# Kernel tuning notes

Hardware: AMD Instinct MI355X
Metric: run time of the kernel (lower is better)

Reference implementation:

```python
import jax, jax.numpy as jnp
import numpy as np

L = 3        # layer_num
D = 64       # hidden_size (input_dim)
NU = 100000  # user nodes in batched graph
NI = 100000  # item nodes in batched graph
NUSER = 200000  # user vocab
NITEM = 200000  # item vocab
E = 1000000  # edges per relation ('by' and 'pby')
B = 1024     # target users per batch


def _time_enc(t, freq, phase):
    # TimeEncode: cos(t * basis_freq + phase), per edge -> [E, D]
    return jnp.cos(t[:, None] * freq[None, :] + phase[None, :])


def _seg_attn(e, vals, dst, num_seg):
    # softmax of e over edges sharing a destination node, then weighted sum of vals
    m = jax.ops.segment_max(e, dst, num_segments=num_seg)
    ex = jnp.exp(e - m[dst])
    denom = jax.ops.segment_sum(ex, dst, num_segments=num_seg)
    alpha = ex / denom[dst]
    return jax.ops.segment_sum(alpha[:, None] * vals, dst, num_segments=num_seg)


def _forward(user_emb, item_emb, Wu, Wi, Wuu, Wii,
             u_freq, u_phase, uk_freq, uk_phase,
             i_freq, i_phase, ik_freq, ik_phase,
             unified_W, dense_W, dense_b,
             by_time, pby_time,
             user_id, item_id, by_src, by_dst, pby_src, pby_dst,
             user_index, last_item_index):
    nu = user_id.shape[0]
    ni = item_id.shape[0]
    d = user_emb.shape[1]
    scale = 1.0 / jnp.sqrt(jnp.float32(d))
    user_h = user_emb[user_id]   # [NU, D]
    item_h = item_emb[item_id]   # [NI, D]
    user_layers = []
    n_layers = Wu.shape[0]
    for l in range(n_layers):
        uh = user_h @ Wu[l]   # user_weight
        ih = item_h @ Wi[l]   # item_weight
        # --- 'by' relation: item -> user (user_reduce_func) ---
        src_i = ih[by_src]    # mailbox['item_h']
        dst_u = uh[by_dst]    # mailbox['user_h'] (dst feature)
        e_u = jnp.sum((_time_enc(by_time, u_freq[l], u_phase[l]) + src_i) * dst_u, -1) * scale
        agg_u = _seg_attn(e_u, src_i + _time_enc(by_time, uk_freq[l], uk_phase[l]), by_dst, nu)
        # --- 'pby' relation: user -> item (item_reduce_func) ---
        src_u = uh[pby_src]
        dst_i = ih[pby_dst]
        e_i = jnp.sum((_time_enc(pby_time, i_freq[l], i_phase[l]) + src_u) * dst_i, -1) * scale
        agg_i = _seg_attn(e_i, src_u + _time_enc(pby_time, ik_freq[l], ik_phase[l]), pby_dst, ni)
        # node update: elu(W [agg ; old])
        user_h = jax.nn.elu(jnp.concatenate([agg_u, user_h], -1) @ Wuu[l])
        item_h = jax.nn.elu(jnp.concatenate([agg_i, item_h], -1) @ Wii[l])
        user_layers.append(user_h[user_index])
    user_layers.append(item_h[last_item_index])  # last_item=True
    unified = jnp.concatenate(user_layers, -1) @ unified_W
    return jax.nn.relu(unified @ dense_W + dense_b)  # [B, 3]


def setup_inputs() -> dict:
    key = jax.random.key(0)
    ks = jax.random.split(key, 20)
    w = lambda k, shape: jax.random.normal(k, shape, jnp.float32) * 0.05
    freq0 = jnp.asarray(1.0 / 10 ** np.linspace(0, 9, D), dtype=jnp.float32)
    freq = jnp.tile(freq0[None], (L, 1))
    zph = jnp.zeros((L, D), jnp.float32)
    return {
        'user_emb': w(ks[0], (NUSER, D)),
        'item_emb': w(ks[1], (NITEM, D)),
        'Wu': w(ks[2], (L, D, D)),
        'Wi': w(ks[3], (L, D, D)),
        'Wuu': w(ks[4], (L, 2 * D, D)),
        'Wii': w(ks[5], (L, 2 * D, D)),
        'u_freq': freq, 'u_phase': zph,
        'uk_freq': freq, 'uk_phase': zph,
        'i_freq': freq, 'i_phase': zph,
        'ik_freq': freq, 'ik_phase': zph,
        'unified_W': w(ks[6], ((L + 1) * D, D)),
        'dense_W': w(ks[7], (D, 3)),
        'dense_b': jnp.zeros((3,), jnp.float32),
        'by_time': jax.random.uniform(ks[8], (E,), jnp.float32),
        'pby_time': jax.random.uniform(ks[9], (E,), jnp.float32),
        'user_id': jax.random.randint(ks[10], (NU,), 0, NUSER),
        'item_id': jax.random.randint(ks[11], (NI,), 0, NITEM),
        'by_src': jax.random.randint(ks[12], (E,), 0, NI),
        'by_dst': jax.random.randint(ks[13], (E,), 0, NU),
        'pby_src': jax.random.randint(ks[14], (E,), 0, NU),
        'pby_dst': jax.random.randint(ks[15], (E,), 0, NI),
        'user_index': jax.random.randint(ks[16], (B,), 0, NU),
        'last_item_index': jax.random.randint(ks[17], (B,), 0, NI),
    }


def reference(user_emb, item_emb, Wu, Wi, Wuu, Wii,
              u_freq, u_phase, uk_freq, uk_phase,
              i_freq, i_phase, ik_freq, ik_phase,
              unified_W, dense_W, dense_b,
              by_time, pby_time,
              user_id, item_id, by_src, by_dst, pby_src, pby_dst,
              user_index, last_item_index):
    return _forward(user_emb, item_emb, Wu, Wi, Wuu, Wii,
                    u_freq, u_phase, uk_freq, uk_phase,
                    i_freq, i_phase, ik_freq, ik_phase,
                    unified_W, dense_W, dense_b,
                    by_time, pby_time,
                    user_id, item_id, by_src, by_dst, pby_src, pby_dst,
                    user_index, last_item_index)
```

## Files before the change

### kernel.cpp

```cpp
#include <hip/hip_runtime.h>
#include <math.h>

#define D 64

typedef __attribute__((ext_vector_type(8))) short s8bf;
typedef __attribute__((ext_vector_type(4))) float fx4;

__device__ __forceinline__ float bf2f(unsigned short u) {
    union { unsigned int i; float f; } v; v.i = ((unsigned int)u) << 16; return v.f;
}
__device__ __forceinline__ unsigned short f2bf(float f) {
    union { float f; unsigned int i; } v; v.f = f;
    unsigned int r = v.i + 0x7FFFu + ((v.i >> 16) & 1u);
    return (unsigned short)(r >> 16);
}

__global__ __launch_bounds__(256) void k_gather2(const float* __restrict__ ue,
                                                 const float* __restrict__ ie,
                                                 const int* __restrict__ uid,
                                                 const int* __restrict__ iid,
                                                 unsigned short* __restrict__ uh0,
                                                 unsigned short* __restrict__ ih0, int NU, int NI) {
    int i = blockIdx.x * blockDim.x + threadIdx.x;
    if (i >= (NU + NI) * D) return;
    int r = i >> 6, c = i & 63;
    if (r < NU) uh0[(size_t)r * D + c] = f2bf(ue[(size_t)uid[r] * D + c]);
    else { int j = r - NU; ih0[(size_t)j * D + c] = f2bf(ie[(size_t)iid[j] * D + c]); }
}

__global__ __launch_bounds__(256) void k_wprep(const float* __restrict__ Wu,
                                               const float* __restrict__ Wi,
                                               const float* __restrict__ Wuu,
                                               const float* __restrict__ Wii,
                                               unsigned short* __restrict__ WuT,
                                               unsigned short* __restrict__ WiT,
                                               unsigned short* __restrict__ WuuT,
                                               unsigned short* __restrict__ WiiT, int L) {
    int i = blockIdx.x * blockDim.x + threadIdx.x;
    int n1 = L * 64 * 64, n2 = L * 64 * 128;
    if (i < n1) {
        int l = i >> 12, c = (i >> 6) & 63, k = i & 63;
        WuT[i] = f2bf(Wu[l * 4096 + k * 64 + c]);
        WiT[i] = f2bf(Wi[l * 4096 + k * 64 + c]);
    }
    if (i < n2) {
        int l = i >> 13, c = (i >> 7) & 63, k = i & 127;
        WuuT[i] = f2bf(Wuu[l * 8192 + k * 64 + c]);
        WiiT[i] = f2bf(Wii[l * 8192 + k * 64 + c]);
    }
}

__global__ __launch_bounds__(256) void k_hist2(const int* __restrict__ bd,
                                               const int* __restrict__ pd,
                                               int* __restrict__ cu, int* __restrict__ ci, int E) {
    for (int i = blockIdx.x * blockDim.x + threadIdx.x; i < 2 * E; i += gridDim.x * blockDim.x) {
        if (i < E) atomicAdd(&cu[bd[i]], 1);
        else       atomicAdd(&ci[pd[i - E]], 1);
    }
}

__global__ __launch_bounds__(256) void k_scan_block2(const int* __restrict__ cu, int* __restrict__ rp_u,
                                                     const int* __restrict__ ci, int* __restrict__ rp_i,
                                                     int* __restrict__ bsums, int nbU, int NU, int NI) {
    __shared__ int ts[256];
    bool rel = blockIdx.x >= (unsigned)nbU;
    const int* in = rel ? ci : cu;
    int* out = rel ? rp_i : rp_u;
    int n = rel ? NI : NU;
    int boff = rel ? blockIdx.x - nbU : blockIdx.x;
    int t = threadIdx.x;
    int base = boff * 2048 + t * 8;
    int v[8]; int s = 0;
#pragma unroll
    for (int k = 0; k < 8; ++k) { int idx = base + k; v[k] = idx < n ? in[idx] : 0; s += v[k]; }
    ts[t] = s; __syncthreads();
    for (int off = 1; off < 256; off <<= 1) {
        int x = (t >= off) ? ts[t - off] : 0;
        __syncthreads(); ts[t] += x; __syncthreads();
    }
    int excl = ts[t] - s;
    if (t == 255) bsums[blockIdx.x] = ts[255];
    int run = excl;
#pragma unroll
    for (int k = 0; k < 8; ++k) { int idx = base + k; if (idx < n) out[idx] = run; run += v[k]; }
}

__global__ __launch_bounds__(256) void k_scan_small(int* __restrict__ bsums, int nbU, int nbI) {
    __shared__ int ts[256];
    int t = threadIdx.x;
    int half = t >> 7, local = t & 127;
    int nb = half ? nbI : nbU;
    int g = half ? nbU + local : local;
    int v = local < nb ? bsums[g] : 0;
    ts[t] = v; __syncthreads();
    for (int off = 1; off < 128; off <<= 1) {
        int x = (local >= off) ? ts[t - off] : 0;
        __syncthreads(); ts[t] += x; __syncthreads();
    }
    if (local < nb) bsums[g] = ts[t] - v;
}

__global__ __launch_bounds__(256) void k_fixup2(int* __restrict__ rp_u, int* __restrict__ rp_i,
                                                const int* __restrict__ bsums,
                                                int* __restrict__ cu, int* __restrict__ ci,
                                                int NU, int NI, int E, int nbU) {
    int i = blockIdx.x * blockDim.x + threadIdx.x;
    if (i < NU) {
        int v = rp_u[i] + bsums[i >> 11]; rp_u[i] = v; cu[i] = v;
        if (i == 0) rp_u[NU] = E;
    } else if (i < NU + NI) {
        int j = i - NU;
        int v = rp_i[j] + bsums[nbU + (j >> 11)]; rp_i[j] = v; ci[j] = v;
        if (j == 0) rp_i[NI] = E;
    }
}

__global__ __launch_bounds__(256) void k_scatter2(
    const int* __restrict__ bs, const int* __restrict__ bd, const float* __restrict__ bt,
    const int* __restrict__ ps, const int* __restrict__ pd, const float* __restrict__ pt,
    int* __restrict__ cu, int* __restrict__ ci,
    int4* __restrict__ be, int4* __restrict__ pe, int E) {
    for (int i = blockIdx.x * blockDim.x + threadIdx.x; i < 2 * E; i += gridDim.x * blockDim.x) {
        if (i < E) {
            int d = bd[i]; int pos = atomicAdd(&cu[d], 1);
            be[pos] = make_int4(bs[i], __float_as_int(bt[i]), d, 0);
        } else {
            int k = i - E;
            int d = pd[k]; int pos = atomicAdd(&ci[d], 1);
            pe[pos] = make_int4(ps[k], __float_as_int(pt[k]), d, 0);
        }
    }
}

__global__ __launch_bounds__(256) void k_transform4(
    const unsigned short* __restrict__ user_h, const unsigned short* __restrict__ item_h,
    const unsigned short* __restrict__ WuT_l, const unsigned short* __restrict__ WiT_l,
    unsigned short* __restrict__ uh, unsigned short* __restrict__ ih,
    int NU, int NI, int G) {
    bool rel = blockIdx.x >= (unsigned)G;
    int b = rel ? blockIdx.x - G : blockIdx.x;
    const unsigned short* in = rel ? item_h : user_h;
    const unsigned short* WT = rel ? WiT_l : WuT_l;
    unsigned short* out = rel ? ih : uh;
    int n = rel ? NI : NU;
    int lane = threadIdx.x & 63;
    int l15 = lane & 15, l4 = lane >> 4;
    s8bf bfr[8];
#pragma unroll
    for (int ct = 0; ct < 4; ++ct)
#pragma unroll
        for (int kk = 0; kk < 2; ++kk)
            bfr[ct * 2 + kk] = *(const s8bf*)&WT[(ct * 16 + l15) * 64 + kk * 32 + l4 * 8];
    int wave = b * 4 + (threadIdx.x >> 6);
    int nw = G * 4;
    int ntiles = (n + 15) >> 4;
    for (int t = wave; t < ntiles; t += nw) {
        int r = t * 16 + l15; if (r >= n) r = n - 1;
        s8bf afr0 = *(const s8bf*)&in[(size_t)r * 64 + l4 * 8];
        s8bf afr1 = *(const s8bf*)&in[(size_t)r * 64 + 32 + l4 * 8];
#pragma unroll
        for (int ct = 0; ct < 4; ++ct) {
            fx4 c = {0.f, 0.f, 0.f, 0.f};
            c = __builtin_amdgcn_mfma_f32_16x16x32_bf16(afr0, bfr[ct * 2 + 0], c, 0, 0, 0);
            c = __builtin_amdgcn_mfma_f32_16x16x32_bf16(afr1, bfr[ct * 2 + 1], c, 0, 0, 0);
#pragma unroll
            for (int i2 = 0; i2 < 4; ++i2) {
                int row = t * 16 + l4 * 4 + i2;
                if (row < n) out[(size_t)row * 64 + ct * 16 + l15] = f2bf(c[i2]);
            }
        }
    }
}

__global__ __launch_bounds__(256) void k_edge2(
    const unsigned short* __restrict__ ihF, const unsigned short* __restrict__ uhF,
    const int4* __restrict__ by_e, const int4* __restrict__ pby_e,
    const float* __restrict__ uf, const float* __restrict__ up,
    const float* __restrict__ ukf, const float* __restrict__ ukp,
    const float* __restrict__ ifq, const float* __restrict__ ipq,
    const float* __restrict__ ikf, const float* __restrict__ ikp,
    float* __restrict__ agg_u, float* __restrict__ den_u,
    float* __restrict__ agg_i, float* __restrict__ den_i,
    int E, int EB) {
    bool rel = blockIdx.x >= (unsigned)EB;
    int rblk = rel ? blockIdx.x - EB : blockIdx.x;
    const unsigned short* srcF = rel ? uhF : ihF;
    const unsigned short* dstF = rel ? ihF : uhF;
    const int4* ee = rel ? pby_e : by_e;
    const float* efq = rel ? ifq : uf;
    const float* eps = rel ? ipq : up;
    const float* kfq = rel ? ikf : ukf;
    const float* kps = rel ? ikp : ukp;
    float* agg = rel ? agg_i : agg_u;
    float* den = rel ? den_i : den_u;

    int lane = threadIdx.x & 15;
    int grp  = threadIdx.x >> 4;
    int base = rblk * 256 + grp * 16;
    if (base >= E) return;
    float ef0 = efq[lane], ef1 = efq[lane + 16], ef2 = efq[lane + 32], ef3 = efq[lane + 48];
    float ep0 = eps[lane], ep1 = eps[lane + 16], ep2 = eps[lane + 32], ep3 = eps[lane + 48];
    float kf0 = kfq[lane], kf1 = kfq[lane + 16], kf2 = kfq[lane + 32], kf3 = kfq[lane + 48];
    float kp0 = kps[lane], kp1 = kps[lane + 16], kp2 = kps[lane + 32], kp3 = kps[lane + 48];
    bool same = ef0 == kf0 && ef1 == kf1 && ef2 == kf2 && ef3 == kf3 &&
                ep0 == kp0 && ep1 == kp1 && ep2 == kp2 && ep3 == kp3;
    same = __all(same);

    float a0 = 0, a1 = 0, a2 = 0, a3 = 0, dn = 0;
    float d0 = 0, d1 = 0, d2 = 0, d3 = 0;
    int cur = -1;
    for (int j = 0; j < 16; ++j) {
        int e = base + j;
        if (e >= E) break;
        int4 q = ee[e];
        int s = q.x; float t = __int_as_float(q.y); int dd = q.z;
        if (dd != cur) {
            if (cur >= 0) {
                float* ap = &agg[(size_t)cur * D + lane];
                unsafeAtomicAdd(ap +  0, a0); unsafeAtomicAdd(ap + 16, a1);
                unsafeAtomicAdd(ap + 32, a2); unsafeAtomicAdd(ap + 48, a3);
                if (lane == 0) unsafeAtomicAdd(&den[cur], dn);
            }
            a0 = a1 = a2 = a3 = 0; dn = 0; cur = dd;
            const unsigned short* dp = &dstF[(size_t)dd * D + lane];
            d0 = bf2f(dp[0]); d1 = bf2f(dp[16]); d2 = bf2f(dp[32]); d3 = bf2f(dp[48]);
        }
        const unsigned short* sp = &srcF[(size_t)s * D + lane];
        float s0 = bf2f(sp[0]), s1 = bf2f(sp[16]), s2 = bf2f(sp[32]), s3 = bf2f(sp[48]);
        float c0 = __cosf(fmaf(t, ef0, ep0));
        float c1 = __cosf(fmaf(t, ef1, ep1));
        float c2 = __cosf(fmaf(t, ef2, ep2));
        float c3 = __cosf(fmaf(t, ef3, ep3));
        float p = (c0 + s0) * d0 + (c1 + s1) * d1 + (c2 + s2) * d2 + (c3 + s3) * d3;
        p += __shfl_xor(p, 1); p += __shfl_xor(p, 2);
        p += __shfl_xor(p, 4); p += __shfl_xor(p, 8);
        float ex = __expf(p * 0.125f);
        float k0, k1, k2, k3;
        if (same) { k0 = c0; k1 = c1; k2 = c2; k3 = c3; }
        else {
            k0 = __cosf(fmaf(t, kf0, kp0)); k1 = __cosf(fmaf(t, kf1, kp1));
            k2 = __cosf(fmaf(t, kf2, kp2)); k3 = __cosf(fmaf(t, kf3, kp3));
        }
        a0 = fmaf(ex, s0 + k0, a0); a1 = fmaf(ex, s1 + k1, a1);
        a2 = fmaf(ex, s2 + k2, a2); a3 = fmaf(ex, s3 + k3, a3);
        dn += ex;
    }
    if (cur >= 0) {
        float* ap = &agg[(size_t)cur * D + lane];
        unsafeAtomicAdd(ap +  0, a0); unsafeAtomicAdd(ap + 16, a1);
        unsafeAtomicAdd(ap + 32, a2); unsafeAtomicAdd(ap + 48, a3);
        if (lane == 0) unsafeAtomicAdd(&den[cur], dn);
    }
}

__global__ __launch_bounds__(256) void k_update4(
    unsigned short* __restrict__ user_h, unsigned short* __restrict__ item_h,
    const float* __restrict__ agg_u, const float* __restrict__ den_u,
    const float* __restrict__ agg_i, const float* __restrict__ den_i,
    const unsigned short* __restrict__ WuuT_l, const unsigned short* __restrict__ WiiT_l,
    int NU, int NI, int G) {
    bool rel = blockIdx.x >= (unsigned)G;
    int b = rel ? blockIdx.x - G : blockIdx.x;
    unsigned short* h = rel ? item_h : user_h;
    const float* agg = rel ? agg_i : agg_u;
    const float* den = rel ? den_i : den_u;
    const unsigned short* WT = rel ? WiiT_l : WuuT_l;
    int n = rel ? NI : NU;
    int lane = threadIdx.x & 63;
    int l15 = lane & 15, l4 = lane >> 4;
    s8bf bfr[16];
#pragma unroll
    for (int ct = 0; ct < 4; ++ct)
#pragma unroll
        for (int kk = 0; kk < 4; ++kk)
            bfr[ct * 4 + kk] = *(const s8bf*)&WT[(ct * 16 + l15) * 128 + kk * 32 + l4 * 8];
    int wave = b * 4 + (threadIdx.x >> 6);
    int nw = G * 4;
    int ntiles = (n + 15) >> 4;
    for (int t = wave; t < ntiles; t += nw) {
        int r = t * 16 + l15; if (r >= n) r = n - 1;
        float dd = den[r];
        float inv = dd > 0.f ? 1.f / dd : 0.f;
        s8bf afr[4];
#pragma unroll
        for (int kk = 0; kk < 2; ++kk) {
            const float4* ap = (const float4*)&agg[(size_t)r * 64 + kk * 32 + l4 * 8];
            float4 x = ap[0], y = ap[1];
            s8bf f;
            f[0] = (short)f2bf(x.x * inv); f[1] = (short)f2bf(x.y * inv);
            f[2] = (short)f2bf(x.z * inv); f[3] = (short)f2bf(x.w * inv);
            f[4] = (short)f2bf(y.x * inv); f[5] = (short)f2bf(y.y * inv);
            f[6] = (short)f2bf(y.z * inv); f[7] = (short)f2bf(y.w * inv);
            afr[kk] = f;
        }
        afr[2] = *(const s8bf*)&h[(size_t)r * 64 + l4 * 8];
        afr[3] = *(const s8bf*)&h[(size_t)r * 64 + 32 + l4 * 8];
#pragma unroll
        for (int ct = 0; ct < 4; ++ct) {
            fx4 c = {0.f, 0.f, 0.f, 0.f};
            c = __builtin_amdgcn_mfma_f32_16x16x32_bf16(afr[0], bfr[ct * 4 + 0], c, 0, 0, 0);
            c = __builtin_amdgcn_mfma_f32_16x16x32_bf16(afr[1], bfr[ct * 4 + 1], c, 0, 0, 0);
            c = __builtin_amdgcn_mfma_f32_16x16x32_bf16(afr[2], bfr[ct * 4 + 2], c, 0, 0, 0);
            c = __builtin_amdgcn_mfma_f32_16x16x32_bf16(afr[3], bfr[ct * 4 + 3], c, 0, 0, 0);
#pragma unroll
            for (int i2 = 0; i2 < 4; ++i2) {
                int row = t * 16 + l4 * 4 + i2;
                if (row < n) {
                    float o = c[i2];
                    h[(size_t)row * 64 + ct * 16 + l15] =
                        f2bf(o > 0.f ? o : __expf(o) - 1.f);
                }
            }
        }
    }
}

__global__ __launch_bounds__(256) void k_gather_feat(const unsigned short* __restrict__ h,
                                                     const int* __restrict__ idx,
                                                     float* __restrict__ feat, int B,
                                                     int colOff, int FW) {
    int i = blockIdx.x * blockDim.x + threadIdx.x;
    if (i >= B * D) return;
    int b = i >> 6, c = i & 63;
    feat[(size_t)b * FW + colOff + c] = bf2f(h[(size_t)idx[b] * D + c]);
}

__global__ __launch_bounds__(64) void k_final(const float* __restrict__ feat,
                                              const float* __restrict__ uW,
                                              const float* __restrict__ dW,
                                              const float* __restrict__ db,
                                              float* __restrict__ out, int B, int FW) {
    __shared__ float fr[512];
    __shared__ float un[D];
    int b = blockIdx.x;
    int c = threadIdx.x;
    for (int i = c; i < FW; i += 64) fr[i] = feat[(size_t)b * FW + i];
    __syncthreads();
    float acc = 0.f;
    for (int d = 0; d < FW; ++d) acc += fr[d] * uW[d * D + c];
    un[c] = acc;
    __syncthreads();
    if (c < 3) {
        float o = db[c];
#pragma unroll
        for (int d = 0; d < D; ++d) o += un[d] * dW[d * 3 + c];
        out[b * 3 + c] = o > 0.f ? o : 0.f;
    }
}

extern "C" void kernel_launch(void* const* d_in, const int* in_sizes, int n_in,
                              void* d_out, int out_size, void* d_ws, size_t ws_size,
                              hipStream_t stream) {
    const float* user_emb = (const float*)d_in[0];
    const float* item_emb = (const float*)d_in[1];
    const float* Wu       = (const float*)d_in[2];
    const float* Wi       = (const float*)d_in[3];
    const float* Wuu      = (const float*)d_in[4];
    const float* Wii      = (const float*)d_in[5];
    const float* u_freq   = (const float*)d_in[6];
    const float* u_phase  = (const float*)d_in[7];
    const float* uk_freq  = (const float*)d_in[8];
    const float* uk_phase = (const float*)d_in[9];
    const float* i_freq   = (const float*)d_in[10];
    const float* i_phase  = (const float*)d_in[11];
    const float* ik_freq  = (const float*)d_in[12];
    const float* ik_phase = (const float*)d_in[13];
    const float* unified_W = (const float*)d_in[14];
    const float* dense_W   = (const float*)d_in[15];
    const float* dense_b   = (const float*)d_in[16];
    const float* by_time   = (const float*)d_in[17];
    const float* pby_time  = (const float*)d_in[18];
    const int* user_id   = (const int*)d_in[19];
    const int* item_id   = (const int*)d_in[20];
    const int* by_src    = (const int*)d_in[21];
    const int* by_dst    = (const int*)d_in[22];
    const int* pby_src   = (const int*)d_in[23];
    const int* pby_dst   = (const int*)d_in[24];
    const int* user_index = (const int*)d_in[25];
    const int* last_item_index = (const int*)d_in[26];

    const int NU = in_sizes[19];
    const int NI = in_sizes[20];
    const int E  = in_sizes[21];
    const int B  = in_sizes[25];
    const int L  = in_sizes[2] / (D * D);
    const int FW = (L + 1) * D;

    char* wp = (char*)d_ws;
    auto alloc_f = [&](size_t n) { float* p = (float*)wp; wp += n * sizeof(float); return p; };
    auto alloc_i = [&](size_t n) { int* p = (int*)wp; wp += n * sizeof(int); return p; };
    auto alloc_i4 = [&](size_t n) { int4* p = (int4*)wp; wp += n * sizeof(int4); return p; };
    auto alloc_h = [&](size_t n) { unsigned short* p = (unsigned short*)wp; wp += n * sizeof(unsigned short); return p; };
    float* agg_u = alloc_f((size_t)NU * D);
    float* agg_i = alloc_f((size_t)NI * D);
    float* den_u = alloc_f(NU);
    float* den_i = alloc_f(NI);
    size_t zero_bytes = (size_t)(wp - (char*)d_ws);
    int4* by_e  = alloc_i4(E);
    int4* pby_e = alloc_i4(E);
    int* cur_u = alloc_i(NU);
    int* cur_i = alloc_i(NI);
    size_t cur_bytes = (size_t)NU * 4 + (size_t)NI * 4;
    unsigned short* user_h = alloc_h((size_t)NU * D);
    unsigned short* item_h = alloc_h((size_t)NI * D);
    unsigned short* uh = alloc_h((size_t)NU * D);
    unsigned short* ih = alloc_h((size_t)NI * D);
    unsigned short* WuT  = alloc_h((size_t)L * 64 * 64);
    unsigned short* WiT  = alloc_h((size_t)L * 64 * 64);
    unsigned short* WuuT = alloc_h((size_t)L * 64 * 128);
    unsigned short* WiiT = alloc_h((size_t)L * 64 * 128);
    int*   by_rowptr  = alloc_i(NU + 2);
    int*   pby_rowptr = alloc_i(NI + 2);
    int*   bsums      = alloc_i(512);
    float* feat       = alloc_f((size_t)B * FW);

    const int nbU = (NU + 2047) / 2048, nbI = (NI + 2047) / 2048;

    k_gather2<<<((NU + NI) * D + 255) / 256, 256, 0, stream>>>(
        user_emb, item_emb, user_id, item_id, user_h, item_h, NU, NI);
    k_wprep<<<(L * 64 * 128 + 255) / 256, 256, 0, stream>>>(Wu, Wi, Wuu, Wii,
                                                            WuT, WiT, WuuT, WiiT, L);

    hipMemsetAsync(cur_u, 0, cur_bytes, stream);
    k_hist2<<<2048, 256, 0, stream>>>(by_dst, pby_dst, cur_u, cur_i, E);
    k_scan_block2<<<nbU + nbI, 256, 0, stream>>>(cur_u, by_rowptr, cur_i, pby_rowptr,
                                                 bsums, nbU, NU, NI);
    k_scan_small<<<1, 256, 0, stream>>>(bsums, nbU, nbI);
    k_fixup2<<<(NU + NI + 255) / 256, 256, 0, stream>>>(by_rowptr, pby_rowptr, bsums,
                                                        cur_u, cur_i, NU, NI, E, nbU);
    k_scatter2<<<2048, 256, 0, stream>>>(by_src, by_dst, by_time,
                                         pby_src, pby_dst, pby_time,
                                         cur_u, cur_i, by_e, pby_e, E);

    const int EB = (E + 255) / 256;
    const int GM = 512;
    for (int l = 0; l < L; ++l) {
        hipMemsetAsync(d_ws, 0, zero_bytes, stream);
        k_transform4<<<2 * GM, 256, 0, stream>>>(user_h, item_h,
                                                 WuT + (size_t)l * 4096, WiT + (size_t)l * 4096,
                                                 uh, ih, NU, NI, GM);
        k_edge2<<<2 * EB, 256, 0, stream>>>(
            ih, uh, by_e, pby_e,
            u_freq + l * D, u_phase + l * D, uk_freq + l * D, uk_phase + l * D,
            i_freq + l * D, i_phase + l * D, ik_freq + l * D, ik_phase + l * D,
            agg_u, den_u, agg_i, den_i, E, EB);
        k_update4<<<2 * GM, 256, 0, stream>>>(user_h, item_h,
                                              agg_u, den_u, agg_i, den_i,
                                              WuuT + (size_t)l * 8192, WiiT + (size_t)l * 8192,
                                              NU, NI, GM);
        k_gather_feat<<<(B * D + 255) / 256, 256, 0, stream>>>(user_h, user_index, feat, B,
                                                               l * D, FW);
    }
    k_gather_feat<<<(B * D + 255) / 256, 256, 0, stream>>>(item_h, last_item_index, feat, B,
                                                           L * D, FW);
    k_final<<<B, 64, 0, stream>>>(feat, unified_W, dense_W, dense_b, (float*)d_out, B, FW);
}
```

Baseline: 740.2 us.

## Two-pass bucketed edge scatter and 32 edges per group in edge kernel

After: 912.7 us. +23.3%, slower.

```diff
diff --git a/kernel.cpp b/kernel.cpp
--- a/kernel.cpp
+++ b/kernel.cpp
@@ -2,6 +2,7 @@
 #include <math.h>
 
 #define D 64
+#define NB 1024
 
 typedef __attribute__((ext_vector_type(8))) short s8bf;
 typedef __attribute__((ext_vector_type(4))) float fx4;
@@ -115,20 +116,65 @@
     }
 }
 
-__global__ __launch_bounds__(256) void k_scatter2(
+__global__ __launch_bounds__(256) void k_binit(const int* __restrict__ rp_u,
+                                               const int* __restrict__ rp_i,
+                                               int* __restrict__ bcu, int* __restrict__ bci,
+                                               int NU, int NI, int npbU, int npbI) {
+    int b = blockIdx.x * blockDim.x + threadIdx.x;
+    if (b >= 2 * NB) return;
+    if (b < NB) {
+        long long s = (long long)b * npbU; if (s > NU) s = NU;
+        bcu[b] = rp_u[s];
+    } else {
+        int bb = b - NB;
+        long long s = (long long)bb * npbI; if (s > NI) s = NI;
+        bci[bb] = rp_i[s];
+    }
+}
+
+__global__ __launch_bounds__(256) void k_bucket(
     const int* __restrict__ bs, const int* __restrict__ bd, const float* __restrict__ bt,
     const int* __restrict__ ps, const int* __restrict__ pd, const float* __restrict__ pt,
-    int* __restrict__ cu, int* __restrict__ ci,
-    int4* __restrict__ be, int4* __restrict__ pe, int E) {
+    int* __restrict__ bcu, int* __restrict__ bci,
+    int4* __restrict__ stg_by, int4* __restrict__ stg_pby,
+    int E, unsigned npbU, unsigned npbI) {
     for (int i = blockIdx.x * blockDim.x + threadIdx.x; i < 2 * E; i += gridDim.x * blockDim.x) {
         if (i < E) {
-            int d = bd[i]; int pos = atomicAdd(&cu[d], 1);
-            be[pos] = make_int4(bs[i], __float_as_int(bt[i]), d, 0);
+            int d = bd[i];
+            unsigned b = (unsigned)d / npbU;
+            int pos = atomicAdd(&bcu[b], 1);
+            stg_by[pos] = make_int4(bs[i], __float_as_int(bt[i]), d, 0);
         } else {
             int k = i - E;
-            int d = pd[k]; int pos = atomicAdd(&ci[d], 1);
-            pe[pos] = make_int4(ps[k], __float_as_int(pt[k]), d, 0);
+            int d = pd[k];
+            unsigned b = (unsigned)d / npbI;
+            int pos = atomicAdd(&bci[b], 1);
+            stg_pby[pos] = make_int4(ps[k], __float_as_int(pt[k]), d, 0);
         }
+    }
+}
+
+__global__ __launch_bounds__(256) void k_sortfin(
+    const int4* __restrict__ stg_by, const int4* __restrict__ stg_pby,
+    const int* __restrict__ rp_u, const int* __restrict__ rp_i,
+    int* __restrict__ cu, int* __restrict__ ci,
+    int4* __restrict__ by_e, int4* __restrict__ pby_e,
+    int NU, int NI, int npbU, int npbI) {
+    bool rel = blockIdx.x >= (unsigned)NB;
+    int b = rel ? blockIdx.x - NB : blockIdx.x;
+    const int4* stg = rel ? stg_pby : stg_by;
+    const int* rp = rel ? rp_i : rp_u;
+    int* cur = rel ? ci : cu;
+    int4* out = rel ? pby_e : by_e;
+    int n = rel ? NI : NU;
+    int npb = rel ? npbI : npbU;
+    long long s0 = (long long)b * npb; if (s0 > n) s0 = n;
+    long long s1 = (long long)(b + 1) * npb; if (s1 > n) s1 = n;
+    int beg = rp[s0], end = rp[s1];
+    for (int j = beg + threadIdx.x; j < end; j += 256) {
+        int4 q = stg[j];
+        int pos = atomicAdd(&cur[q.z], 1);
+        out[pos] = q;
     }
 }
 
@@ -196,7 +242,7 @@
 
     int lane = threadIdx.x & 15;
     int grp  = threadIdx.x >> 4;
-    int base = rblk * 256 + grp * 16;
+    int base = rblk * 512 + grp * 32;
     if (base >= E) return;
     float ef0 = efq[lane], ef1 = efq[lane + 16], ef2 = efq[lane + 32], ef3 = efq[lane + 48];
     float ep0 = eps[lane], ep1 = eps[lane + 16], ep2 = eps[lane + 32], ep3 = eps[lane + 48];
@@ -209,7 +255,7 @@
     float a0 = 0, a1 = 0, a2 = 0, a3 = 0, dn = 0;
     float d0 = 0, d1 = 0, d2 = 0, d3 = 0;
     int cur = -1;
-    for (int j = 0; j < 16; ++j) {
+    for (int j = 0; j < 32; ++j) {
         int e = base + j;
         if (e >= E) break;
         int4 q = ee[e];
@@ -385,6 +431,8 @@
     const int B  = in_sizes[25];
     const int L  = in_sizes[2] / (D * D);
     const int FW = (L + 1) * D;
+    const int npbU = (NU + NB - 1) / NB;
+    const int npbI = (NI + NB - 1) / NB;
 
     char* wp = (char*)d_ws;
     auto alloc_f = [&](size_t n) { float* p = (float*)wp; wp += n * sizeof(float); return p; };
@@ -396,8 +444,10 @@
     float* den_u = alloc_f(NU);
     float* den_i = alloc_f(NI);
     size_t zero_bytes = (size_t)(wp - (char*)d_ws);
-    int4* by_e  = alloc_i4(E);
-    int4* pby_e = alloc_i4(E);
+    int4* by_e    = alloc_i4(E);
+    int4* pby_e   = alloc_i4(E);
+    int4* stg_by  = alloc_i4(E);
+    int4* stg_pby = alloc_i4(E);
     int* cur_u = alloc_i(NU);
     int* cur_i = alloc_i(NI);
     size_t cur_bytes = (size_t)NU * 4 + (size_t)NI * 4;
@@ -412,6 +462,8 @@
     int*   by_rowptr  = alloc_i(NU + 2);
     int*   pby_rowptr = alloc_i(NI + 2);
     int*   bsums      = alloc_i(512);
+    int*   bcur_u     = alloc_i(NB);
+    int*   bcur_i     = alloc_i(NB);
     float* feat       = alloc_f((size_t)B * FW);
 
     const int nbU = (NU + 2047) / 2048, nbI = (NI + 2047) / 2048;
@@ -428,11 +480,17 @@
     k_scan_small<<<1, 256, 0, stream>>>(bsums, nbU, nbI);
     k_fixup2<<<(NU + NI + 255) / 256, 256, 0, stream>>>(by_rowptr, pby_rowptr, bsums,
                                                         cur_u, cur_i, NU, NI, E, nbU);
-    k_scatter2<<<2048, 256, 0, stream>>>(by_src, by_dst, by_time,
-                                         pby_src, pby_dst, pby_time,
-                                         cur_u, cur_i, by_e, pby_e, E);
-
-    const int EB = (E + 255) / 256;
+    k_binit<<<(2 * NB + 255) / 256, 256, 0, stream>>>(by_rowptr, pby_rowptr,
+                                                      bcur_u, bcur_i, NU, NI, npbU, npbI);
+    k_bucket<<<2048, 256, 0, stream>>>(by_src, by_dst, by_time,
+                                       pby_src, pby_dst, pby_time,
+                                       bcur_u, bcur_i, stg_by, stg_pby,
+                                       E, (unsigned)npbU, (unsigned)npbI);
+    k_sortfin<<<2 * NB, 256, 0, stream>>>(stg_by, stg_pby, by_rowptr, pby_rowptr,
+                                          cur_u, cur_i, by_e, pby_e,
+                                          NU, NI, npbU, npbI);
+
+    const int EB = (E + 511) / 512;
     const int GM = 512;
     for (int l = 0; l < L; ++l) {
         hipMemsetAsync(d_ws, 0, zero_bytes, stream);
```

## Replace atomic edge scatter with two-pass bucketed partition for locality

Applied to the files above, without the earlier changes.

New measurement: 697.3 us. 5.8% less time.

```diff
diff --git a/kernel.cpp b/kernel.cpp
--- a/kernel.cpp
+++ b/kernel.cpp
@@ -2,9 +2,12 @@
 #include <math.h>
 
 #define D 64
+#define NB 1024
+#define CHUNKE 4096
 
 typedef __attribute__((ext_vector_type(8))) short s8bf;
 typedef __attribute__((ext_vector_type(4))) float fx4;
+typedef __attribute__((ext_vector_type(4))) int ix4;
 
 __device__ __forceinline__ float bf2f(unsigned short u) {
     union { unsigned int i; float f; } v; v.i = ((unsigned int)u) << 16; return v.f;
@@ -115,20 +118,120 @@
     }
 }
 
-__global__ __launch_bounds__(256) void k_scatter2(
+__global__ __launch_bounds__(256) void k_phist(const int* __restrict__ bd,
+                                               const int* __restrict__ pd,
+                                               int* __restrict__ H, int E, int nwgE,
+                                               unsigned npbU, unsigned npbI) {
+    bool rel = blockIdx.x >= (unsigned)nwgE;
+    int wg = rel ? blockIdx.x - nwgE : blockIdx.x;
+    const int* dsts = rel ? pd : bd;
+    unsigned npb = rel ? npbI : npbU;
+    int* Hr = H + (rel ? NB * nwgE : 0);
+    __shared__ int hist[NB];
+    int t = threadIdx.x;
+    for (int j = t; j < NB; j += 256) hist[j] = 0;
+    __syncthreads();
+    int base = wg * CHUNKE;
+#pragma unroll
+    for (int k = 0; k < CHUNKE / 256; ++k) {
+        int e = base + t + k * 256;
+        if (e < E) atomicAdd(&hist[(unsigned)dsts[e] / npb], 1);
+    }
+    __syncthreads();
+    for (int j = t; j < NB; j += 256) Hr[j * nwgE + wg] = hist[j];
+}
+
+__global__ __launch_bounds__(256) void k_gscan_block(const int* __restrict__ in,
+                                                     int* __restrict__ out,
+                                                     int* __restrict__ bsums, int n) {
+    __shared__ int ts[256];
+    int t = threadIdx.x;
+    int base = blockIdx.x * 2048 + t * 8;
+    int v[8]; int s = 0;
+#pragma unroll
+    for (int k = 0; k < 8; ++k) { int idx = base + k; v[k] = idx < n ? in[idx] : 0; s += v[k]; }
+    ts[t] = s; __syncthreads();
+    for (int off = 1; off < 256; off <<= 1) {
+        int x = (t >= off) ? ts[t - off] : 0;
+        __syncthreads(); ts[t] += x; __syncthreads();
+    }
+    int excl = ts[t] - s;
+    if (t == 255) bsums[blockIdx.x] = ts[255];
+    int run = excl;
+#pragma unroll
+    for (int k = 0; k < 8; ++k) { int idx = base + k; if (idx < n) out[idx] = run; run += v[k]; }
+}
+
+__global__ __launch_bounds__(256) void k_gscan_small(int* __restrict__ bsums, int nb) {
+    __shared__ int ts[256];
+    int t = threadIdx.x;
+    int v = t < nb ? bsums[t] : 0;
+    ts[t] = v; __syncthreads();
+    for (int off = 1; off < 256; off <<= 1) {
+        int x = (t >= off) ? ts[t - off] : 0;
+        __syncthreads(); ts[t] += x; __syncthreads();
+    }
+    if (t < nb) bsums[t] = ts[t] - v;
+}
+
+__global__ __launch_bounds__(256) void k_gscan_fix(int* __restrict__ out,
+                                                   const int* __restrict__ bsums, int n) {
+    int i = blockIdx.x * blockDim.x + threadIdx.x;
+    if (i < n) out[i] += bsums[i >> 11];
+}
+
+__global__ __launch_bounds__(256) void k_ppart(
     const int* __restrict__ bs, const int* __restrict__ bd, const float* __restrict__ bt,
     const int* __restrict__ ps, const int* __restrict__ pd, const float* __restrict__ pt,
+    const int* __restrict__ H, ix4* __restrict__ stg_by, ix4* __restrict__ stg_pby,
+    int E, int nwgE, unsigned npbU, unsigned npbI) {
+    bool rel = blockIdx.x >= (unsigned)nwgE;
+    int wg = rel ? blockIdx.x - nwgE : blockIdx.x;
+    const int* srcs = rel ? ps : bs;
+    const int* dsts = rel ? pd : bd;
+    const float* tms = rel ? pt : bt;
+    unsigned npb = rel ? npbI : npbU;
+    const int* Hr = H + (rel ? NB * nwgE : 0);
+    ix4* stg = rel ? stg_pby : stg_by;
+    int sub = rel ? E : 0;
+    __shared__ int cur[NB];
+    int t = threadIdx.x;
+    for (int j = t; j < NB; j += 256) cur[j] = Hr[j * nwgE + wg] - sub;
+    __syncthreads();
+    int base = wg * CHUNKE;
+#pragma unroll
+    for (int k = 0; k < CHUNKE / 256; ++k) {
+        int e = base + t + k * 256;
+        if (e < E) {
+            int d = dsts[e];
+            int pos = atomicAdd(&cur[(unsigned)d / npb], 1);
+            ix4 v = {srcs[e], __float_as_int(tms[e]), d, 0};
+            stg[pos] = v;
+        }
+    }
+}
+
+__global__ __launch_bounds__(256) void k_sortfin(
+    const ix4* __restrict__ stg_by, const ix4* __restrict__ stg_pby,
+    const int* __restrict__ rp_u, const int* __restrict__ rp_i,
     int* __restrict__ cu, int* __restrict__ ci,
-    int4* __restrict__ be, int4* __restrict__ pe, int E) {
-    for (int i = blockIdx.x * blockDim.x + threadIdx.x; i < 2 * E; i += gridDim.x * blockDim.x) {
-        if (i < E) {
-            int d = bd[i]; int pos = atomicAdd(&cu[d], 1);
-            be[pos] = make_int4(bs[i], __float_as_int(bt[i]), d, 0);
-        } else {
-            int k = i - E;
-            int d = pd[k]; int pos = atomicAdd(&ci[d], 1);
-            pe[pos] = make_int4(ps[k], __float_as_int(pt[k]), d, 0);
-        }
+    ix4* __restrict__ by_e, ix4* __restrict__ pby_e,
+    int NU, int NI, int npbU, int npbI) {
+    bool rel = blockIdx.x >= (unsigned)NB;
+    int b = rel ? blockIdx.x - NB : blockIdx.x;
+    const ix4* stg = rel ? stg_pby : stg_by;
+    const int* rp = rel ? rp_i : rp_u;
+    int* cur = rel ? ci : cu;
+    ix4* out = rel ? pby_e : by_e;
+    int n = rel ? NI : NU;
+    int npb = rel ? npbI : npbU;
+    long long s0 = (long long)b * npb; if (s0 > n) s0 = n;
+    long long s1 = (long long)(b + 1) * npb; if (s1 > n) s1 = n;
+    int beg = rp[s0], end = rp[s1];
+    for (int j = beg + threadIdx.x; j < end; j += 256) {
+        ix4 q = stg[j];
+        int pos = atomicAdd(&cur[q.z], 1);
+        out[pos] = q;
     }
 }
 
@@ -174,7 +277,7 @@
 
 __global__ __launch_bounds__(256) void k_edge2(
     const unsigned short* __restrict__ ihF, const unsigned short* __restrict__ uhF,
-    const int4* __restrict__ by_e, const int4* __restrict__ pby_e,
+    const ix4* __restrict__ by_e, const ix4* __restrict__ pby_e,
     const float* __restrict__ uf, const float* __restrict__ up,
     const float* __restrict__ ukf, const float* __restrict__ ukp,
     const float* __restrict__ ifq, const float* __restrict__ ipq,
@@ -186,7 +289,7 @@
     int rblk = rel ? blockIdx.x - EB : blockIdx.x;
     const unsigned short* srcF = rel ? uhF : ihF;
     const unsigned short* dstF = rel ? ihF : uhF;
-    const int4* ee = rel ? pby_e : by_e;
+    const ix4* ee = rel ? pby_e : by_e;
     const float* efq = rel ? ifq : uf;
     const float* eps = rel ? ipq : up;
     const float* kfq = rel ? ikf : ukf;
@@ -212,7 +315,7 @@
     for (int j = 0; j < 16; ++j) {
         int e = base + j;
         if (e >= E) break;
-        int4 q = ee[e];
+        ix4 q = ee[e];
         int s = q.x; float t = __int_as_float(q.y); int dd = q.z;
         if (dd != cur) {
             if (cur >= 0) {
@@ -385,19 +488,24 @@
     const int B  = in_sizes[25];
     const int L  = in_sizes[2] / (D * D);
     const int FW = (L + 1) * D;
+    const int npbU = (NU + NB - 1) / NB;
+    const int npbI = (NI + NB - 1) / NB;
+    const int nwgE = (E + CHUNKE - 1) / CHUNKE;
 
     char* wp = (char*)d_ws;
     auto alloc_f = [&](size_t n) { float* p = (float*)wp; wp += n * sizeof(float); return p; };
     auto alloc_i = [&](size_t n) { int* p = (int*)wp; wp += n * sizeof(int); return p; };
-    auto alloc_i4 = [&](size_t n) { int4* p = (int4*)wp; wp += n * sizeof(int4); return p; };
+    auto alloc_i4 = [&](size_t n) { ix4* p = (ix4*)wp; wp += n * sizeof(ix4); return p; };
     auto alloc_h = [&](size_t n) { unsigned short* p = (unsigned short*)wp; wp += n * sizeof(unsigned short); return p; };
     float* agg_u = alloc_f((size_t)NU * D);
     float* agg_i = alloc_f((size_t)NI * D);
     float* den_u = alloc_f(NU);
     float* den_i = alloc_f(NI);
     size_t zero_bytes = (size_t)(wp - (char*)d_ws);
-    int4* by_e  = alloc_i4(E);
-    int4* pby_e = alloc_i4(E);
+    ix4* by_e    = alloc_i4(E);
+    ix4* pby_e   = alloc_i4(E);
+    ix4* stg_by  = alloc_i4(E);
+    ix4* stg_pby = alloc_i4(E);
     int* cur_u = alloc_i(NU);
     int* cur_i = alloc_i(NI);
     size_t cur_bytes = (size_t)NU * 4 + (size_t)NI * 4;
@@ -412,6 +520,8 @@
     int*   by_rowptr  = alloc_i(NU + 2);
     int*   pby_rowptr = alloc_i(NI + 2);
     int*   bsums      = alloc_i(512);
+    int*   H          = alloc_i((size_t)2 * NB * nwgE);
+    int*   gbsums     = alloc_i(512);
     float* feat       = alloc_f((size_t)B * FW);
 
     const int nbU = (NU + 2047) / 2048, nbI = (NI + 2047) / 2048;
@@ -428,9 +538,23 @@
     k_scan_small<<<1, 256, 0, stream>>>(bsums, nbU, nbI);
     k_fixup2<<<(NU + NI + 255) / 256, 256, 0, stream>>>(by_rowptr, pby_rowptr, bsums,
                                                         cur_u, cur_i, NU, NI, E, nbU);
-    k_scatter2<<<2048, 256, 0, stream>>>(by_src, by_dst, by_time,
-                                         pby_src, pby_dst, pby_time,
-                                         cur_u, cur_i, by_e, pby_e, E);
+
+    k_phist<<<2 * nwgE, 256, 0, stream>>>(by_dst, pby_dst, H, E, nwgE,
+                                          (unsigned)npbU, (unsigned)npbI);
+    {
+        int n2 = 2 * NB * nwgE;
+        int gb = (n2 + 2047) / 2048;
+        k_gscan_block<<<gb, 256, 0, stream>>>(H, H, gbsums, n2);
+        k_gscan_small<<<1, 256, 0, stream>>>(gbsums, gb);
+        k_gscan_fix<<<(n2 + 255) / 256, 256, 0, stream>>>(H, gbsums, n2);
+    }
+    k_ppart<<<2 * nwgE, 256, 0, stream>>>(by_src, by_dst, by_time,
+                                          pby_src, pby_dst, pby_time,
+                                          H, stg_by, stg_pby, E, nwgE,
+                                          (unsigned)npbU, (unsigned)npbI);
+    k_sortfin<<<2 * NB, 256, 0, stream>>>(stg_by, stg_pby, by_rowptr, pby_rowptr,
+                                          cur_u, cur_i, by_e, pby_e,
+                                          NU, NI, npbU, npbI);
 
     const int EB = (E + 255) / 256;
     const int GM = 512;
```
